# Performance work log

Hardware: AMD Instinct MI355X
Metric: run time of the kernel (lower is better)

Reference implementation:

```python
import jax, jax.numpy as jnp
import numpy as np

N = 10000
E = 160000
F_IN = 2000
HEADS = 10
C1 = 128      # layer-1 per-head out channels
C2 = 128      # layer-2 per-head out channels (latent_dim)
NEG_SLOPE = 0.2
EPS = 1e-16


def gat_conv(x, W, att_src, att_dst, bias, src, dst, heads, out_ch, concat):
    """PyG-style GATConv (eval mode, self-loops already included in src/dst).
    x: [N, F_in]; W: [F_in, heads*out_ch]; att_*: [heads, out_ch]; bias: [out_dim].
    src/dst: [E'] edge endpoints (message flows src -> dst).
    """
    n = x.shape[0]
    h = (x @ W).reshape(n, heads, out_ch)              # [N, H, C]
    a_src = jnp.einsum('nhc,hc->nh', h, att_src)       # [N, H]
    a_dst = jnp.einsum('nhc,hc->nh', h, att_dst)       # [N, H]
    e = a_src[src] + a_dst[dst]                        # [E', H]
    e = jax.nn.leaky_relu(e, NEG_SLOPE)
    # segment softmax over incoming edges of each destination node
    m = jax.ops.segment_max(e, dst, num_segments=n)    # [N, H]
    ex = jnp.exp(e - m[dst])
    s = jax.ops.segment_sum(ex, dst, num_segments=n)   # [N, H]
    alpha = ex / (s[dst] + EPS)                        # [E', H]
    msg = h[src] * alpha[:, :, None]                   # [E', H, C]
    out = jax.ops.segment_sum(msg, dst, num_segments=n)  # [N, H, C]
    out = out.reshape(n, heads * out_ch) if concat else out.mean(axis=1)
    return out + bias


def setup_inputs() -> dict:
    key = jax.random.key(0)
    ks = jax.random.split(key, 10)
    glorot = lambda k, shape: jax.random.normal(k, shape, jnp.float32) * np.sqrt(2.0 / (shape[0] + shape[-1]))
    x = jax.random.normal(ks[0], (N, F_IN), jnp.float32)
    edge_index = jax.random.randint(ks[1], (2, E), 0, N, jnp.int64)
    W1 = glorot(ks[2], (F_IN, HEADS * C1))
    att_src1 = glorot(ks[3], (HEADS, C1))
    att_dst1 = glorot(ks[4], (HEADS, C1))
    b1 = jnp.zeros((HEADS * C1,), jnp.float32)
    W2 = glorot(ks[5], (HEADS * C1, HEADS * C2))
    att_src2 = glorot(ks[6], (HEADS, C2))
    att_dst2 = glorot(ks[7], (HEADS, C2))
    b2 = jnp.zeros((C2,), jnp.float32)
    return dict(x=x, edge_index=edge_index, W1=W1, att_src1=att_src1,
                att_dst1=att_dst1, b1=b1, W2=W2, att_src2=att_src2,
                att_dst2=att_dst2, b2=b2)


def reference(x, edge_index, W1, att_src1, att_dst1, b1, W2, att_src2, att_dst2, b2):
    n = x.shape[0]
    loops = jnp.arange(n, dtype=edge_index.dtype)
    src = jnp.concatenate([edge_index[0], loops])  # add self-loops (PyG default)
    dst = jnp.concatenate([edge_index[1], loops])
    h = jax.nn.relu(gat_conv(x, W1, att_src1, att_dst1, b1, src, dst, HEADS, C1, True))
    z = jax.nn.relu(gat_conv(h, W2, att_src2, att_dst2, b2, src, dst, HEADS, C2, False))
    return z
```

## Files before the change

### kernel.cpp

```cpp
#include <hip/hip_runtime.h>

typedef unsigned short u16;
typedef __attribute__((ext_vector_type(8))) short bf16x8;
typedef __attribute__((ext_vector_type(4))) float f32x4;
typedef __attribute__((ext_vector_type(4))) unsigned u32x4;

#define NN    10000
#define EE    160000
#define ET    170000
#define FIN   2000
#define MPAD  10112
#define K1PAD 2048
#define NH    1280
#define HEADS 10
#define NT    10
#define NWG2  395

__device__ __forceinline__ u16 f32_to_bf16(float f) {
    unsigned u = __float_as_uint(f);
    unsigned r = (u + 0x7fffu + ((u >> 16) & 1u)) >> 16;
    return (u16)r;
}
__device__ __forceinline__ float bf16lo(unsigned pv) { return __uint_as_float(pv << 16); }
__device__ __forceinline__ float bf16hi(unsigned pv) { return __uint_as_float(pv & 0xffff0000u); }

__device__ __forceinline__ void gload16(const u16* g, u16* l) {
    __builtin_amdgcn_global_load_lds(
        (const __attribute__((address_space(1))) void*)g,
        (__attribute__((address_space(3))) void*)l, 16, 0, 0);
}

__global__ __launch_bounds__(256) void k_prep(const float* __restrict__ x,
                                              uint2* __restrict__ A1,
                                              const float* __restrict__ W1,
                                              u16* __restrict__ B1t) {
    __shared__ float tile[32][33];
    const int bid = blockIdx.x;
    const int t = threadIdx.x;
    if (bid < 2048) {
        const int total = MPAD * (K1PAD / 4);
        for (int idx = bid * 256 + t; idx < total; idx += 2048 * 256) {
            int r = idx >> 9;
            int c = (idx & 511) << 2;
            float4 v = make_float4(0.f, 0.f, 0.f, 0.f);
            if (r < NN && c < FIN) v = *(const float4*)(x + (size_t)r * FIN + c);
            uint2 p;
            p.x = (unsigned)f32_to_bf16(v.x) | ((unsigned)f32_to_bf16(v.y) << 16);
            p.y = (unsigned)f32_to_bf16(v.z) | ((unsigned)f32_to_bf16(v.w) << 16);
            A1[idx] = p;
        }
        return;
    }
    const int tx = t & 31, ty = t >> 5;
    int b = bid - 2048;
    int k0 = (b & 63) * 32, n0 = (b >> 6) * 32;
    #pragma unroll
    for (int i = 0; i < 32; i += 8) {
        int k = k0 + ty + i;
        tile[ty + i][tx] = (k < FIN) ? W1[(size_t)k * NH + n0 + tx] : 0.f;
    }
    __syncthreads();
    #pragma unroll
    for (int i = 0; i < 32; i += 8) {
        int n = n0 + ty + i, k = k0 + tx;
        B1t[(size_t)n * K1PAD + k] = f32_to_bf16(tile[tx][ty + i]);
    }
}

__global__ __launch_bounds__(256) void k_prepW2(const float* __restrict__ W2,
                                                u16* __restrict__ B2t) {
    __shared__ float tile[32][33];
    const int t = threadIdx.x;
    const int tx = t & 31, ty = t >> 5;
    int b = blockIdx.x;
    int k0 = (b % 40) * 32, n0 = (b / 40) * 32;
    #pragma unroll
    for (int i = 0; i < 32; i += 8)
        tile[ty + i][tx] = W2[(size_t)(k0 + ty + i) * NH + n0 + tx];
    __syncthreads();
    #pragma unroll
    for (int i = 0; i < 32; i += 8) {
        int n = n0 + ty + i, k = k0 + tx;
        B2t[(size_t)n * NH + k] = f32_to_bf16(tile[tx][ty + i]);
    }
}

__global__ __launch_bounds__(512) void k_gemm(const u16* __restrict__ A,
                                              const u16* __restrict__ Bt,
                                              u16* __restrict__ Chm,
                                              const int Kpad, const int kTiles) {
    __shared__ __attribute__((aligned(16))) u16 S[32768];
    const int bid = blockIdx.x;
    const int xcd = bid & 7, idx = bid >> 3;
    const int q = NWG2 >> 3, rr = NWG2 & 7;
    const int P = (xcd < rr) ? (xcd * (q + 1) + idx)
                             : (rr * (q + 1) + (xcd - rr) * q + idx);
    const int L0 = 2 * P;
    const size_t m0 = (size_t)(L0 / NT) * 128;
    const int n0a = (L0 % NT) * 128;

    const int t = threadIdx.x;
    const int lane = t & 63;
    const int wave = t >> 6;
    const int wr = wave >> 2, wc = wave & 3;

    f32x4 acc[4][2] = {};

    const int srow = t >> 3;
    const int klocal = (((t & 7) ^ ((t >> 3) & 7)) << 3);
    const u16* aRow = A + (m0 + srow) * (size_t)Kpad + klocal;
    const u16* bRow = Bt + (size_t)(n0a + srow) * Kpad + klocal;
    const size_t rStep = (size_t)64 * Kpad;
    const size_t bTile = (size_t)128 * Kpad;

#define STAGE(j_, bufb_) do {                                                    \
        char* db = (char*)S + (bufb_) + wave * 1024;                             \
        const int jj_ = (j_) < kTiles ? (j_) : (j_) - kTiles;                    \
        const u16* bR_ = (j_) < kTiles ? bRow : bRow + bTile;                    \
        const u16* aP = aRow + (size_t)jj_ * 64;                                 \
        const u16* bP = bR_ + (size_t)jj_ * 64;                                  \
        gload16(aP,         (u16*)(db));                                         \
        gload16(aP + rStep, (u16*)(db + 8192));                                  \
        gload16(bP,         (u16*)(db + 16384));                                 \
        gload16(bP + rStep, (u16*)(db + 24576));                                 \
    } while (0)

#define EPILOG(ncol_) do {                                                       \
        u16* Cb_ = Chm + (size_t)((ncol_) >> 7) * (MPAD << 7);                   \
        _Pragma("unroll")                                                        \
        for (int mf_ = 0; mf_ < 4; ++mf_)                                        \
            _Pragma("unroll")                                                    \
            for (int i_ = 0; i_ < 4; ++i_) {                                     \
                size_t row_ = m0 + wr * 64 + mf_ * 16 + (lane >> 4) * 4 + i_;    \
                u16* crow_ = Cb_ + row_ * 128 + wc * 32 + (lane & 15);           \
                _Pragma("unroll")                                                \
                for (int nf_ = 0; nf_ < 2; ++nf_)                                \
                    crow_[nf_ * 16] = f32_to_bf16(acc[mf_][nf_][i_]);            \
            }                                                                    \
    } while (0)

    STAGE(0, 0);

    const int rl = lane & 15;
    const int kchunk = lane >> 4;
    const int xorv = (rl & 7) << 4;
    const int aBase0 = (wr * 64 + rl) * 128;
    const int bBase0 = (wc * 32 + rl) * 128;
    const char* Sb = (const char*)S;
    const int kTotal = 2 * kTiles;

    for (int kt = 0; kt < kTotal; ++kt) {
        asm volatile("s_waitcnt vmcnt(0)" ::: "memory");
        __builtin_amdgcn_s_barrier();
        if (kt + 1 < kTotal) STAGE(kt + 1, ((kt + 1) & 1) * 32768);
        const int bufo = (kt & 1) * 32768;
        #pragma unroll
        for (int ks = 0; ks < 2; ++ks) {
            const int px = (ks * 64 + kchunk * 16) ^ xorv;
            bf16x8 af[4], bfr[2];
            #pragma unroll
            for (int mf = 0; mf < 4; ++mf)
                af[mf] = *(const bf16x8*)(Sb + bufo + aBase0 + mf * 2048 + px);
            #pragma unroll
            for (int nf = 0; nf < 2; ++nf)
                bfr[nf] = *(const bf16x8*)(Sb + bufo + 16384 + bBase0 + nf * 2048 + px);
            #pragma unroll
            for (int mf = 0; mf < 4; ++mf)
                #pragma unroll
                for (int nf = 0; nf < 2; ++nf)
                    acc[mf][nf] = __builtin_amdgcn_mfma_f32_16x16x32_bf16(
                        af[mf], bfr[nf], acc[mf][nf], 0, 0, 0);
        }
        if (kt == kTiles - 1) {
            EPILOG(n0a);
            #pragma unroll
            for (int mf = 0; mf < 4; ++mf)
                #pragma unroll
                for (int nf = 0; nf < 2; ++nf)
                    acc[mf][nf] = (f32x4){0.f, 0.f, 0.f, 0.f};
        }
    }
    EPILOG(n0a + 128);
#undef STAGE
#undef EPILOG
}

__global__ __launch_bounds__(256) void k_attn(const u16* __restrict__ Hhm,
                                              const float* __restrict__ att_s,
                                              const float* __restrict__ att_d,
                                              float* __restrict__ a_src,
                                              float* __restrict__ a_dst) {
    const int lane = threadIdx.x & 63;
    const int n = blockIdx.x * 4 + (threadIdx.x >> 6);
    if (n >= NN) return;
    const unsigned* Hd = (const unsigned*)Hhm;
    #pragma unroll
    for (int h = 0; h < HEADS; ++h) {
        unsigned pv = Hd[((size_t)h * MPAD + n) * 64 + lane];
        float v0 = bf16lo(pv), v1 = bf16hi(pv);
        int c = h * 128 + lane * 2;
        float s = v0 * att_s[c] + v1 * att_s[c + 1];
        float d = v0 * att_d[c] + v1 * att_d[c + 1];
        #pragma unroll
        for (int o = 32; o; o >>= 1) { s += __shfl_xor(s, o); d += __shfl_xor(d, o); }
        if (lane == 0) { a_src[h * NN + n] = s; a_dst[h * NN + n] = d; }
    }
}

__global__ void k_count(const int* __restrict__ ei, int* __restrict__ deg) {
    int e = blockIdx.x * blockDim.x + threadIdx.x;
    if (e >= ET) return;
    int d = (e < EE) ? ei[EE + e] : (e - EE);
    atomicAdd(&deg[d], 1);
}

__global__ __launch_bounds__(1024) void k_scan(const int* __restrict__ deg,
                                               int* __restrict__ off,
                                               int* __restrict__ cursor) {
    __shared__ int wt[16];
    const int t = threadIdx.x, lane = t & 63, w = t >> 6;
    const int lo = t * 10;
    const int hi = (lo + 10 < NN) ? lo + 10 : NN;
    int s = 0;
    for (int i = lo; i < hi; ++i) s += deg[i];
    int x = s;
    #pragma unroll
    for (int o = 1; o < 64; o <<= 1) { int y = __shfl_up(x, o); if (lane >= o) x += y; }
    if (lane == 63) wt[w] = x;
    __syncthreads();
    int wp = 0;
    for (int k = 0; k < w; ++k) wp += wt[k];
    int run = wp + x - s;
    for (int i = lo; i < hi; ++i) { off[i] = run; cursor[i] = run; run += deg[i]; }
    if (t == 1023) off[NN] = wp + x;
}

__global__ void k_scatter(const int* __restrict__ ei, int* __restrict__ cursor,
                          int* __restrict__ csr_src) {
    int e = blockIdx.x * blockDim.x + threadIdx.x;
    if (e >= ET) return;
    int s = (e < EE) ? ei[e] : (e - EE);
    int d = (e < EE) ? ei[EE + e] : (e - EE);
    int pos = atomicAdd(&cursor[d], 1);
    csr_src[pos] = s;
}

template <int LAYER>
__global__ __launch_bounds__(256) void k_agg(const u16* __restrict__ Hhm,
                                             const float* __restrict__ a_src,
                                             const float* __restrict__ a_dst,
                                             const int* __restrict__ off,
                                             const int* __restrict__ csr,
                                             const float* __restrict__ bias,
                                             unsigned* __restrict__ outp) {
    const int bid = blockIdx.x;
    if (LAYER == 1 && bid >= 6256) {
        int idx = (bid - 6256) * 256 + threadIdx.x;
        if (idx < 112 * 640) outp[(size_t)NN * 640 + idx] = 0u;
        return;
    }
    const int xcd = bid & 7, slot = bid >> 3;
    const int wv = threadIdx.x >> 6, lane = threadIdx.x & 63;
    const int u = slot * 4 + wv;
    if (u >= 3125) return;
    int h, qd;
    if (u < 2500) { h = xcd; qd = u; }
    else {
        int qg = xcd * 625 + (u - 2500);
        h = 8 + (qg >= 2500);
        qd = (qg >= 2500) ? qg - 2500 : qg;
    }
    const int g = lane >> 4, l = lane & 15;
    const int n = qd * 4 + g;
    const int beg = off[n], end = off[n + 1];
    const u16* Hh = Hhm + (size_t)h * (MPAD * 128);
    const float* asl = a_src + (size_t)h * NN;
    const float ad = a_dst[(size_t)h * NN + n];

    float acc[8] = {};
    float den = 0.f;
    int i = beg;
    for (; i + 3 < end; i += 4) {
        const int s0 = csr[i], s1 = csr[i + 1], s2 = csr[i + 2], s3 = csr[i + 3];
        const float a0 = asl[s0], a1 = asl[s1], a2 = asl[s2], a3 = asl[s3];
        const u32x4 v0 = *(const u32x4*)(Hh + (size_t)s0 * 128 + l * 8);
        const u32x4 v1 = *(const u32x4*)(Hh + (size_t)s1 * 128 + l * 8);
        const u32x4 v2 = *(const u32x4*)(Hh + (size_t)s2 * 128 + l * 8);
        const u32x4 v3 = *(const u32x4*)(Hh + (size_t)s3 * 128 + l * 8);
        float e0 = a0 + ad; e0 = (e0 >= 0.f) ? e0 : 0.2f * e0;
        float e1 = a1 + ad; e1 = (e1 >= 0.f) ? e1 : 0.2f * e1;
        float e2 = a2 + ad; e2 = (e2 >= 0.f) ? e2 : 0.2f * e2;
        float e3 = a3 + ad; e3 = (e3 >= 0.f) ? e3 : 0.2f * e3;
        const float w0 = __expf(e0), w1 = __expf(e1);
        const float w2 = __expf(e2), w3 = __expf(e3);
        den += (w0 + w1) + (w2 + w3);
        #pragma unroll
        for (int j = 0; j < 4; ++j) {
            acc[2 * j]     = fmaf(bf16lo(v0[j]), w0, acc[2 * j]);
            acc[2 * j + 1] = fmaf(bf16hi(v0[j]), w0, acc[2 * j + 1]);
            acc[2 * j]     = fmaf(bf16lo(v1[j]), w1, acc[2 * j]);
            acc[2 * j + 1] = fmaf(bf16hi(v1[j]), w1, acc[2 * j + 1]);
            acc[2 * j]     = fmaf(bf16lo(v2[j]), w2, acc[2 * j]);
            acc[2 * j + 1] = fmaf(bf16hi(v2[j]), w2, acc[2 * j + 1]);
            acc[2 * j]     = fmaf(bf16lo(v3[j]), w3, acc[2 * j]);
            acc[2 * j + 1] = fmaf(bf16hi(v3[j]), w3, acc[2 * j + 1]);
        }
    }
    for (; i < end; ++i) {
        const int s0 = csr[i];
        float e0 = asl[s0] + ad; e0 = (e0 >= 0.f) ? e0 : 0.2f * e0;
        const float w0 = __expf(e0);
        const u32x4 v0 = *(const u32x4*)(Hh + (size_t)s0 * 128 + l * 8);
        den += w0;
        #pragma unroll
        for (int j = 0; j < 4; ++j) {
            acc[2 * j]     = fmaf(bf16lo(v0[j]), w0, acc[2 * j]);
            acc[2 * j + 1] = fmaf(bf16hi(v0[j]), w0, acc[2 * j + 1]);
        }
    }
    const float si = 1.f / (den + 1e-16f);

    u32x4 pk;
    if (LAYER == 1) {
        const int c = h * 128 + l * 8;
        #pragma unroll
        for (int j = 0; j < 4; ++j) {
            float v0 = fmaxf(fmaf(acc[2 * j],     si, bias[c + 2 * j]),     0.f);
            float v1 = fmaxf(fmaf(acc[2 * j + 1], si, bias[c + 2 * j + 1]), 0.f);
            pk[j] = (unsigned)f32_to_bf16(v0) | ((unsigned)f32_to_bf16(v1) << 16);
        }
        *(u32x4*)(outp + (size_t)n * 640 + h * 64 + l * 4) = pk;
    } else {
        #pragma unroll
        for (int j = 0; j < 4; ++j) {
            pk[j] = (unsigned)f32_to_bf16(acc[2 * j] * si)
                  | ((unsigned)f32_to_bf16(acc[2 * j + 1] * si) << 16);
        }
        *(u32x4*)(outp + (size_t)h * (MPAD * 64) + (size_t)n * 64 + l * 4) = pk;
    }
}

__global__ __launch_bounds__(256) void k_final(const unsigned* __restrict__ Z,
                                               const float* __restrict__ b2,
                                               float* __restrict__ out) {
    int t = blockIdx.x * 256 + threadIdx.x;
    if (t >= NN * 64) return;
    int n = t >> 6, d = t & 63;
    float s0 = 0.f, s1 = 0.f;
    #pragma unroll
    for (int h = 0; h < HEADS; ++h) {
        unsigned pv = Z[(size_t)h * (MPAD * 64) + (size_t)n * 64 + d];
        s0 += bf16lo(pv);
        s1 += bf16hi(pv);
    }
    float2 z;
    z.x = fmaxf(fmaf(s0, 0.1f, b2[2 * d]),     0.f);
    z.y = fmaxf(fmaf(s1, 0.1f, b2[2 * d + 1]), 0.f);
    *(float2*)(out + (size_t)n * 128 + 2 * d) = z;
}

extern "C" void kernel_launch(void* const* d_in, const int* in_sizes, int n_in,
                              void* d_out, int out_size, void* d_ws, size_t ws_size,
                              hipStream_t stream) {
    const float* x   = (const float*)d_in[0];
    const int*   ei  = (const int*)  d_in[1];
    const float* W1  = (const float*)d_in[2];
    const float* as1 = (const float*)d_in[3];
    const float* ad1 = (const float*)d_in[4];
    const float* b1  = (const float*)d_in[5];
    const float* W2  = (const float*)d_in[6];
    const float* as2 = (const float*)d_in[7];
    const float* ad2 = (const float*)d_in[8];
    const float* b2  = (const float*)d_in[9];

    char* ws = (char*)d_ws;
    const size_t A1_OFF  = 0;
    const size_t A2_OFF  = 0;
    const size_t B2T_OFF = (size_t)MPAD * NH * 2;
    const size_t H_OFF   = (size_t)MPAD * K1PAD * 2;
    const size_t B1T_OFF = H_OFF + (size_t)MPAD * NH * 2;
    size_t o = B1T_OFF + (size_t)NH * K1PAD * 2;
    const size_t AS_OFF  = o; o += 400128;
    const size_t AD_OFF  = o; o += 400128;
    const size_t DEG_OFF = o; o += 40064;
    const size_t OFF_OFF = o; o += 40064;
    const size_t CUR_OFF = o; o += 40064;
    const size_t CSR_OFF = o; o += 680064;
    if (ws_size < o) return;

    u16*      A1   = (u16*)(ws + A1_OFF);
    unsigned* A2   = (unsigned*)(ws + A2_OFF);
    u16*      B2t  = (u16*)(ws + B2T_OFF);
    u16*      H    = (u16*)(ws + H_OFF);
    u16*      B1t  = (u16*)(ws + B1T_OFF);
    float*    aS   = (float*)(ws + AS_OFF);
    float*    aD   = (float*)(ws + AD_OFF);
    int*      deg  = (int*)(ws + DEG_OFF);
    int*      offp = (int*)(ws + OFF_OFF);
    int*      cur  = (int*)(ws + CUR_OFF);
    int*      csr  = (int*)(ws + CSR_OFF);

    hipMemsetAsync(deg, 0, NN * sizeof(int), stream);
    k_count<<<(ET + 255) / 256, 256, 0, stream>>>(ei, deg);
    k_scan<<<1, 1024, 0, stream>>>(deg, offp, cur);
    k_scatter<<<(ET + 255) / 256, 256, 0, stream>>>(ei, cur, csr);

    k_prep<<<4608, 256, 0, stream>>>(x, (uint2*)A1, W1, B1t);

    k_gemm<<<NWG2, 512, 0, stream>>>(A1, B1t, H, K1PAD, K1PAD / 64);
    k_prepW2<<<1600, 256, 0, stream>>>(W2, B2t);
    k_attn<<<2500, 256, 0, stream>>>(H, as1, ad1, aS, aD);
    k_agg<1><<<6536, 256, 0, stream>>>(H, aS, aD, offp, csr, b1, A2);

    k_gemm<<<NWG2, 512, 0, stream>>>((u16*)A2, B2t, H, NH, NH / 64);
    k_attn<<<2500, 256, 0, stream>>>(H, as2, ad2, aS, aD);
    k_agg<2><<<6256, 256, 0, stream>>>(H, aS, aD, offp, csr, b2, A2);
    k_final<<<(NN * 64 + 255) / 256, 256, 0, stream>>>(A2, b2, (float*)d_out);
}
```

Before: 268.2 us.

## Split GEMM tile staging into two K-halves with partial vmcnt waits

The GEMM main loop's global-to-LDS staging is split by K-half. Each half is issued before the matching compute sub-step, and partial s_waitcnt vmcnt(4) replaces the full drain, so the next tile's loads overlap the current tile's MFMA work at a finer grain. It adds an extra barrier per iteration and moves the staging at the tile boundary after the first epilogue. Correctness depends on the per-thread vmcnt accounting and the buffer reuse ordering holding.

```diff
diff --git a/kernel.cpp b/kernel.cpp
--- a/kernel.cpp
+++ b/kernel.cpp
@@ -108,21 +108,41 @@
 
     const int srow = t >> 3;
     const int klocal = (((t & 7) ^ ((t >> 3) & 7)) << 3);
+    const bool h0t = (klocal < 32);
     const u16* aRow = A + (m0 + srow) * (size_t)Kpad + klocal;
     const u16* bRow = Bt + (size_t)(n0a + srow) * Kpad + klocal;
     const size_t rStep = (size_t)64 * Kpad;
     const size_t bTile = (size_t)128 * Kpad;
 
-#define STAGE(j_, bufb_) do {                                                    \
-        char* db = (char*)S + (bufb_) + wave * 1024;                             \
-        const int jj_ = (j_) < kTiles ? (j_) : (j_) - kTiles;                    \
-        const u16* bR_ = (j_) < kTiles ? bRow : bRow + bTile;                    \
-        const u16* aP = aRow + (size_t)jj_ * 64;                                 \
-        const u16* bP = bR_ + (size_t)jj_ * 64;                                  \
-        gload16(aP,         (u16*)(db));                                         \
-        gload16(aP + rStep, (u16*)(db + 8192));                                  \
-        gload16(bP,         (u16*)(db + 16384));                                 \
-        gload16(bP + rStep, (u16*)(db + 24576));                                 \
+#define STAGE_H(j_, bufb_, half_) do {                                           \
+        if (((half_) == 0) == h0t) {                                             \
+            char* db = (char*)S + (bufb_) + wave * 1024;                         \
+            const int jj_ = (j_) < kTiles ? (j_) : (j_) - kTiles;                \
+            const u16* bR_ = (j_) < kTiles ? bRow : bRow + bTile;                \
+            const u16* aP = aRow + (size_t)jj_ * 64;                             \
+            const u16* bP = bR_ + (size_t)jj_ * 64;                              \
+            gload16(aP,         (u16*)(db));                                     \
+            gload16(aP + rStep, (u16*)(db + 8192));                              \
+            gload16(bP,         (u16*)(db + 16384));                             \
+            gload16(bP + rStep, (u16*)(db + 24576));                             \
+        }                                                                        \
+    } while (0)
+
+#define COMPUTE(ks_, bufo_) do {                                                 \
+        const int px_ = ((ks_) * 64 + kchunk * 16) ^ xorv;                       \
+        bf16x8 af_[4], bfr_[2];                                                  \
+        _Pragma("unroll")                                                        \
+        for (int mf_ = 0; mf_ < 4; ++mf_)                                        \
+            af_[mf_] = *(const bf16x8*)(Sb + (bufo_) + aBase0 + mf_ * 2048 + px_);\
+        _Pragma("unroll")                                                        \
+        for (int nf_ = 0; nf_ < 2; ++nf_)                                        \
+            bfr_[nf_] = *(const bf16x8*)(Sb + (bufo_) + 16384 + bBase0 + nf_ * 2048 + px_);\
+        _Pragma("unroll")                                                        \
+        for (int mf_ = 0; mf_ < 4; ++mf_)                                        \
+            _Pragma("unroll")                                                    \
+            for (int nf_ = 0; nf_ < 2; ++nf_)                                    \
+                acc[mf_][nf_] = __builtin_amdgcn_mfma_f32_16x16x32_bf16(         \
+                    af_[mf_], bfr_[nf_], acc[mf_][nf_], 0, 0, 0);                \
     } while (0)
 
 #define EPILOG(ncol_) do {                                                       \
@@ -139,8 +159,6 @@
             }                                                                    \
     } while (0)
 
-    STAGE(0, 0);
-
     const int rl = lane & 15;
     const int kchunk = lane >> 4;
     const int xorv = (rl & 7) << 4;
@@ -149,28 +167,22 @@
     const char* Sb = (const char*)S;
     const int kTotal = 2 * kTiles;
 
+    STAGE_H(0, 0, 0);
+    STAGE_H(0, 0, 1);
+
     for (int kt = 0; kt < kTotal; ++kt) {
-        asm volatile("s_waitcnt vmcnt(0)" ::: "memory");
+        const int bufn = ((kt + 1) & 1) * 32768;
+        const int bufo = (kt & 1) * 32768;
+        const bool stage_now = (kt + 1 < kTotal) && (kt != kTiles - 1);
+        asm volatile("s_waitcnt vmcnt(4)" ::: "memory");
         __builtin_amdgcn_s_barrier();
-        if (kt + 1 < kTotal) STAGE(kt + 1, ((kt + 1) & 1) * 32768);
-        const int bufo = (kt & 1) * 32768;
-        #pragma unroll
-        for (int ks = 0; ks < 2; ++ks) {
-            const int px = (ks * 64 + kchunk * 16) ^ xorv;
-            bf16x8 af[4], bfr[2];
-            #pragma unroll
-            for (int mf = 0; mf < 4; ++mf)
-                af[mf] = *(const bf16x8*)(Sb + bufo + aBase0 + mf * 2048 + px);
-            #pragma unroll
-            for (int nf = 0; nf < 2; ++nf)
-                bfr[nf] = *(const bf16x8*)(Sb + bufo + 16384 + bBase0 + nf * 2048 + px);
-            #pragma unroll
-            for (int mf = 0; mf < 4; ++mf)
-                #pragma unroll
-                for (int nf = 0; nf < 2; ++nf)
-                    acc[mf][nf] = __builtin_amdgcn_mfma_f32_16x16x32_bf16(
-                        af[mf], bfr[nf], acc[mf][nf], 0, 0, 0);
-        }
+        if (stage_now) STAGE_H(kt + 1, bufn, 0);
+        COMPUTE(0, bufo);
+        if (stage_now) asm volatile("s_waitcnt vmcnt(4)" ::: "memory");
+        else           asm volatile("s_waitcnt vmcnt(0)" ::: "memory");
+        __builtin_amdgcn_s_barrier();
+        if (stage_now) STAGE_H(kt + 1, bufn, 1);
+        COMPUTE(1, bufo);
         if (kt == kTiles - 1) {
             EPILOG(n0a);
             #pragma unroll
@@ -178,10 +190,13 @@
                 #pragma unroll
                 for (int nf = 0; nf < 2; ++nf)
                     acc[mf][nf] = (f32x4){0.f, 0.f, 0.f, 0.f};
+            STAGE_H(kt + 1, bufn, 0);
+            STAGE_H(kt + 1, bufn, 1);
         }
     }
     EPILOG(n0a + 128);
-#undef STAGE
+#undef STAGE_H
+#undef COMPUTE
 #undef EPILOG
 }
 
```

After: 353.5 us. 31.8% more time.
